# Kernel tuning notes

Hardware: AMD Instinct MI355X
Metric: run time of the kernel (lower is better)

## Reference

```python
import jax, jax.numpy as jnp
import numpy as np

B, T, N, F, E, K, H = 512, 48, 62, 5, 496, 3, 512
EPS = 1e-5


def setup_inputs() -> dict:
    key = jax.random.key(0)
    ks = jax.random.split(key, 12)
    x = jax.random.normal(ks[0], (B, T, N, F), jnp.float32)
    edge_src = jax.random.randint(ks[1], (B, E), 0, N)
    edge_dst = jax.random.randint(ks[2], (B, E), 0, N)
    edge_weight = jax.random.uniform(ks[3], (B, E), jnp.float32)
    # ChebConv weights: K linear maps (F->F) + bias, one set per time step t
    Wc = jax.random.normal(ks[4], (T, K, F, F), jnp.float32) * 0.3
    bc = jnp.zeros((T, F), jnp.float32)
    bn_gamma = jnp.ones((T, F), jnp.float32)
    bn_beta = jnp.zeros((T, F), jnp.float32)
    s = 1.0 / np.sqrt(H)
    W_ih = jax.random.uniform(ks[5], (4 * H, N * F), jnp.float32, -s, s)
    W_hh = jax.random.uniform(ks[6], (4 * H, H), jnp.float32, -s, s)
    b_ih = jax.random.uniform(ks[7], (4 * H,), jnp.float32, -s, s)
    b_hh = jax.random.uniform(ks[8], (4 * H,), jnp.float32, -s, s)
    bn1_gamma = jnp.ones((T,), jnp.float32)
    bn1_beta = jnp.zeros((T,), jnp.float32)
    Wl = jax.random.normal(ks[9], (3, H * T), jnp.float32) * 0.02
    bl = jnp.zeros((3,), jnp.float32)
    return dict(x=x, edge_src=edge_src, edge_dst=edge_dst, edge_weight=edge_weight,
                Wc=Wc, bc=bc, bn_gamma=bn_gamma, bn_beta=bn_beta,
                W_ih=W_ih, W_hh=W_hh, b_ih=b_ih, b_hh=b_hh,
                bn1_gamma=bn1_gamma, bn1_beta=bn1_beta, Wl=Wl, bl=bl)


def reference(x, edge_src, edge_dst, edge_weight, Wc, bc, bn_gamma, bn_beta,
              W_ih, W_hh, b_ih, b_hh, bn1_gamma, bn1_beta, Wl, bl):
    # ---- build dense per-graph adjacency (N=62 is tiny, dense is the fast form) ----
    b_idx = jnp.arange(B)[:, None]
    A = jnp.zeros((B, N, N), x.dtype).at[b_idx, edge_dst, edge_src].add(edge_weight)
    deg = A.sum(axis=-1)                      # (B, N) weighted in-degree
    safe = jnp.where(deg > 0, deg, 1.0)
    dinv = jnp.where(deg > 0, 1.0, 0.0) * jax.lax.rsqrt(safe)
    # scaled Laplacian with lambda_max=2 (PyG sym default): L_hat = -D^-1/2 A D^-1/2
    Lhat = -(dinv[:, :, None] * A * dinv[:, None, :])  # (B, N, N)

    # ---- ChebConv per time step, vectorized over T (per-t weights) ----
    xt = jnp.transpose(x, (1, 0, 2, 3))       # (T, B, N, F)
    Tx0 = xt
    out = jnp.einsum('tbnf,tfg->tbng', Tx0, Wc[:, 0])
    Tx1 = jnp.einsum('bnm,tbmf->tbnf', Lhat, Tx0)
    if K > 1:
        out = out + jnp.einsum('tbnf,tfg->tbng', Tx1, Wc[:, 1])
    for k in range(2, K):
        Tx2 = 2.0 * jnp.einsum('bnm,tbmf->tbnf', Lhat, Tx1) - Tx0
        out = out + jnp.einsum('tbnf,tfg->tbng', Tx2, Wc[:, k])
        Tx0, Tx1 = Tx1, Tx2
    out = out + bc[:, None, None, :]

    # ---- BatchNorm over all nodes in the batch (per t, per feature), training stats ----
    mu = out.mean(axis=(1, 2), keepdims=True)
    var = out.var(axis=(1, 2), keepdims=True)
    out = (out - mu) * jax.lax.rsqrt(var + EPS)
    out = out * bn_gamma[:, None, None, :] + bn_beta[:, None, None, :]

    # ---- reshape to LSTM sequence: (B, T, N*F) ----
    seq = jnp.transpose(out, (1, 0, 2, 3)).reshape(B, T, N * F)

    # ---- LSTM (torch gate order i,f,g,o) ----
    def step(carry, x_t):
        h, c = carry
        g = x_t @ W_ih.T + b_ih + h @ W_hh.T + b_hh
        i, f, gg, o = jnp.split(g, 4, axis=-1)
        c = jax.nn.sigmoid(f) * c + jax.nn.sigmoid(i) * jnp.tanh(gg)
        h = jax.nn.sigmoid(o) * jnp.tanh(c)
        return (h, c), h

    h0 = jnp.zeros((B, H), x.dtype)
    _, ys = jax.lax.scan(step, (h0, h0), jnp.transpose(seq, (1, 0, 2)))
    y = jnp.transpose(ys, (1, 0, 2))          # (B, T, H)

    # ---- BatchNorm1d with C=T channels: normalize over (B, H) per t ----
    mu1 = y.mean(axis=(0, 2), keepdims=True)
    var1 = y.var(axis=(0, 2), keepdims=True)
    y = (y - mu1) * jax.lax.rsqrt(var1 + EPS)
    y = y * bn1_gamma[None, :, None] + bn1_beta[None, :, None]

    # ---- head ----
    y = y.reshape(B, T * H)
    return y @ Wl.T + bl
```

## Files before the change

kernel.cpp:

```cpp
#include <hip/hip_runtime.h>
#include <hip/hip_bf16.h>
#include <cstdint>

#define B_ 512
#define T_ 48
#define N_ 62
#define F_ 5
#define E_ 496
#define H_ 512
#define NF_ 310
#define SEQP 320
#define KPAD 832
#define G4 2048
#define EPS_ 1e-5f
#define TC 12
#define LSTR 72

typedef __attribute__((ext_vector_type(8))) short short8;
typedef __attribute__((ext_vector_type(4))) short s16x4;
typedef __attribute__((ext_vector_type(4))) float f32x4;

__device__ __forceinline__ float sigm(float x)  { return 1.f / (1.f + __expf(-x)); }
__device__ __forceinline__ float tanhf_(float x){ return 2.f / (1.f + __expf(-2.f*x)) - 1.f; }

__device__ __forceinline__ short f2b(float v) {
  unsigned int u = __builtin_bit_cast(unsigned int, v);
  unsigned int r = (u + 0x7fffu + ((u >> 16) & 1u)) >> 16;
  return (short)r;
}
__device__ __forceinline__ float b2f(short s) {
  unsigned int u = ((unsigned int)(unsigned short)s) << 16;
  return __builtin_bit_cast(float, u);
}

__device__ __forceinline__ void dma16(const void* g, void* l) {
  __builtin_amdgcn_global_load_lds(
      (const __attribute__((address_space(1))) unsigned int*)g,
      (__attribute__((address_space(3))) unsigned int*)l, 16, 0, 0);
}

__global__ __launch_bounds__(256) void k_lapprep(
    const int* __restrict__ esrc, const int* __restrict__ edst, const float* __restrict__ ew,
    const float* __restrict__ Wih, const float* __restrict__ Whh,
    const float* __restrict__ bih, const float* __restrict__ bhh,
    __hip_bfloat16* __restrict__ lap,
    __hip_bfloat16* __restrict__ Wcat, float* __restrict__ biasr)
{
  const int bid = blockIdx.x;
  const int tid = threadIdx.x;
  __shared__ float Af[N_*N_];
  __shared__ float dinv[N_];

  if (bid < B_) {
    for (int i = tid; i < N_*N_; i += 256) Af[i] = 0.f;
    __syncthreads();
    for (int e = tid; e < E_; e += 256)
      atomicAdd(&Af[edst[bid*E_ + e]*N_ + esrc[bid*E_ + e]], ew[bid*E_ + e]);
    __syncthreads();
    if (tid < N_) {
      float s = 0.f;
      for (int m = 0; m < N_; ++m) s += Af[tid*N_ + m];
      dinv[tid] = (s > 0.f) ? rsqrtf(s) : 0.f;
    }
    __syncthreads();
    short* lp = (short*)lap + (size_t)bid*4096;
    for (int i = tid; i < 4096; i += 256) {
      int n = i >> 6, m = i & 63;
      float v = (n < N_ && m < N_) ? -dinv[n]*Af[n*N_ + m]*dinv[m] : 0.f;
      lp[i] = f2b(v);
    }
  } else {
    const int jp = bid - B_;
    const int g = jp & 3, jh = jp >> 2;
    const int jo = g*H_ + jh;
    for (int k = tid; k < KPAD; k += 256) {
      float v = 0.f;
      if (k < NF_) v = Wih[(size_t)jo*NF_ + k];
      else if (k >= SEQP) v = Whh[(size_t)jo*H_ + (k - SEQP)];
      Wcat[(size_t)jp*KPAD + k] = __float2bfloat16(v);
    }
    if (tid == 0) biasr[jp] = bih[jo] + bhh[jo];
  }
}

__global__ __launch_bounds__(512) void k_cheb(
    const float* __restrict__ x, const __hip_bfloat16* __restrict__ lap,
    const float* __restrict__ Wc, const float* __restrict__ bc,
    float* __restrict__ cheb, float* __restrict__ bps, float* __restrict__ bpq)
{
  __shared__ __align__(16) short SH[4*64*LSTR];
  short* Lb  = SH;
  short* Xt  = SH + 64*LSTR;
  short* T1t = SH + 2*64*LSTR;
  short* T2t = SH + 3*64*LSTR;

  const int tid = threadIdx.x;
  const int b = blockIdx.x;
  const int t0 = blockIdx.y * TC;

  {
    const short8* lp = (const short8*)((const short*)lap + (size_t)b*4096);
    short8 v = lp[tid];
    int n = tid >> 3, m = (tid & 7)*8;
    *(short8*)(Lb + n*LSTR + m) = v;
  }
  for (int i = tid; i < 64*LSTR; i += 512) Xt[i] = 0;
  __syncthreads();

  for (int i = tid; i < TC*NF_; i += 512) {
    int tl = i / NF_, nf = i - tl*NF_;
    float v = x[((size_t)b*T_ + t0 + tl)*NF_ + nf];
    int n = nf / F_, f = nf - n*F_;
    Xt[(tl*F_ + f)*LSTR + n] = f2b(v);
  }
  __syncthreads();

  const int w = tid >> 6, lane = tid & 63, l16 = lane & 15, lhi = lane >> 4;
  const int mt = w >> 1;
  const int nt = (w & 1) * 2;

  {
    f32x4 acc0 = {0.f,0.f,0.f,0.f}, acc1 = acc0;
    #pragma unroll
    for (int kc = 0; kc < 2; ++kc) {
      short8 a  = *(const short8*)(Lb + (mt*16 + l16)*LSTR + kc*32 + lhi*8);
      short8 b0 = *(const short8*)(Xt + ((nt  )*16 + l16)*LSTR + kc*32 + lhi*8);
      short8 b1 = *(const short8*)(Xt + ((nt+1)*16 + l16)*LSTR + kc*32 + lhi*8);
      acc0 = __builtin_amdgcn_mfma_f32_16x16x32_bf16(a, b0, acc0, 0, 0, 0);
      acc1 = __builtin_amdgcn_mfma_f32_16x16x32_bf16(a, b1, acc1, 0, 0, 0);
    }
    #pragma unroll
    for (int i = 0; i < 2; ++i) {
      f32x4 acc = i ? acc1 : acc0;
      int c = (nt+i)*16 + l16, n = mt*16 + lhi*4;
      s16x4 pk;
      #pragma unroll
      for (int r = 0; r < 4; ++r) pk[r] = f2b(acc[r]);
      *(s16x4*)(T1t + c*LSTR + n) = pk;
    }
  }
  __syncthreads();

  {
    f32x4 acc0 = {0.f,0.f,0.f,0.f}, acc1 = acc0;
    #pragma unroll
    for (int kc = 0; kc < 2; ++kc) {
      short8 a  = *(const short8*)(Lb + (mt*16 + l16)*LSTR + kc*32 + lhi*8);
      short8 b0 = *(const short8*)(T1t + ((nt  )*16 + l16)*LSTR + kc*32 + lhi*8);
      short8 b1 = *(const short8*)(T1t + ((nt+1)*16 + l16)*LSTR + kc*32 + lhi*8);
      acc0 = __builtin_amdgcn_mfma_f32_16x16x32_bf16(a, b0, acc0, 0, 0, 0);
      acc1 = __builtin_amdgcn_mfma_f32_16x16x32_bf16(a, b1, acc1, 0, 0, 0);
    }
    #pragma unroll
    for (int i = 0; i < 2; ++i) {
      f32x4 acc = i ? acc1 : acc0;
      int c = (nt+i)*16 + l16, n = mt*16 + lhi*4;
      s16x4 xv = *(const s16x4*)(Xt + c*LSTR + n);
      s16x4 pk;
      #pragma unroll
      for (int r = 0; r < 4; ++r) pk[r] = f2b(2.f*acc[r] - b2f(xv[r]));
      *(s16x4*)(T2t + c*LSTR + n) = pk;
    }
  }
  __syncthreads();

  const int pair = tid >> 2, q = tid & 3;
  if (pair < TC*F_) {
    const int tl = pair / F_, g = pair - (pair/F_)*F_;
    const int t = t0 + tl;
    float w0[5], w1[5], w2[5];
    #pragma unroll
    for (int ff = 0; ff < 5; ++ff) {
      w0[ff] = Wc[t*75 +      ff*5 + g];
      w1[ff] = Wc[t*75 + 25 + ff*5 + g];
      w2[ff] = Wc[t*75 + 50 + ff*5 + g];
    }
    const float bias = bc[t*F_ + g];
    float ss = 0.f, qq = 0.f;
    float* chout = cheb + ((size_t)t*B_ + b)*NF_;
    #pragma unroll
    for (int grp = 0; grp < 4; ++grp) {
      int n4 = grp*16 + q*4;
      float o[4] = {bias, bias, bias, bias};
      #pragma unroll
      for (int ff = 0; ff < 5; ++ff) {
        int c = tl*F_ + ff;
        s16x4 xv = *(const s16x4*)(Xt  + c*LSTR + n4);
        s16x4 v1 = *(const s16x4*)(T1t + c*LSTR + n4);
        s16x4 v2 = *(const s16x4*)(T2t + c*LSTR + n4);
        #pragma unroll
        for (int i = 0; i < 4; ++i)
          o[i] += b2f(xv[i])*w0[ff] + b2f(v1[i])*w1[ff] + b2f(v2[i])*w2[ff];
      }
      #pragma unroll
      for (int i = 0; i < 4; ++i) {
        int n = n4 + i;
        if (n < N_) { chout[n*F_ + g] = o[i]; ss += o[i]; qq += o[i]*o[i]; }
      }
    }
    ss += __shfl_down(ss, 2, 4); ss += __shfl_down(ss, 1, 4);
    qq += __shfl_down(qq, 2, 4); qq += __shfl_down(qq, 1, 4);
    if (q == 0) { bps[(t*F_ + g)*B_ + b] = ss; bpq[(t*F_ + g)*B_ + b] = qq; }
  }
}

__global__ __launch_bounds__(64) void k_bnfin(
    const float* __restrict__ bps, const float* __restrict__ bpq,
    const float* __restrict__ bng, const float* __restrict__ bnb,
    float* __restrict__ alpha, float* __restrict__ bet)
{
  const int tf = blockIdx.x;
  const int lane = threadIdx.x;
  float s = 0.f, q = 0.f;
  for (int i = lane; i < B_; i += 64) { s += bps[tf*B_ + i]; q += bpq[tf*B_ + i]; }
  #pragma unroll
  for (int off = 32; off; off >>= 1) { s += __shfl_down(s, off); q += __shfl_down(q, off); }
  if (lane == 0) {
    const float cnt = (float)(B_*N_);
    float mu = s / cnt;
    float var = q / cnt - mu*mu;
    float al = bng[tf] * rsqrtf(var + EPS_);
    alpha[tf] = al;
    bet[tf] = bnb[tf] - mu*al;
  }
}

__global__ __launch_bounds__(256) void k_seq(
    const float* __restrict__ cheb, const float* __restrict__ alpha, const float* __restrict__ bet,
    __hip_bfloat16* __restrict__ seqb)
{
  int idx = blockIdx.x*256 + threadIdx.x;
  int kp = idx % SEQP;
  int tb = idx / SEQP;
  int b = tb & (B_-1), t = tb >> 9;
  int sl = (kp >> 3) ^ (b & 7);
  int kl = sl*8 + (kp & 7);
  float v = 0.f;
  if (kl < NF_) v = cheb[(size_t)tb*NF_ + kl] * alpha[t*F_ + (kl % F_)] + bet[t*F_ + (kl % F_)];
  seqb[idx] = __float2bfloat16(v);
}

#define WOP(M)  M(0) M(1) M(2) M(3) M(4) M(5) M(6) M(7) M(8) M(9) M(10) M(11) M(12) M(13) \
                M(14) M(15) M(16) M(17) M(18) M(19) M(20) M(21) M(22) M(23) M(24) M(25)
#define WSEQ(M) M(0) M(1) M(2) M(3) M(4) M(5) M(6) M(7) M(8) M(9)
#define WHP(M)  M(10) M(11) M(12) M(13) M(14) M(15) M(16) M(17) M(18) M(19) M(20) M(21) \
                M(22) M(23) M(24) M(25)

#define DECLW(i) short8 wv##i;
#define LOADW(i) wv##i = *(const short8*)(wp + (i)*32); \
                 asm volatile("" : "+v"(wv##i));
#define MFS(i) { const int ph = (((i)*4 + lhi) ^ key)*8; \
                 short8 x0 = *(const short8*)(lseq + rs0*SEQP + ph); \
                 short8 x1 = *(const short8*)(lseq + rs1*SEQP + ph); \
                 a0 = __builtin_amdgcn_mfma_f32_16x16x32_bf16(x0, wv##i, a0, 0, 0, 0); \
                 a1 = __builtin_amdgcn_mfma_f32_16x16x32_bf16(x1, wv##i, a1, 0, 0, 0); }
#define MFH(i) { const int ph = ((((i)-10)*4 + lhi) ^ key)*8; \
                 short8 x0 = *(const short8*)(lh + rs0*H_ + ph); \
                 short8 x1 = *(const short8*)(lh + rs1*H_ + ph); \
                 a0 = __builtin_amdgcn_mfma_f32_16x16x32_bf16(x0, wv##i, a0, 0, 0, 0); \
                 a1 = __builtin_amdgcn_mfma_f32_16x16x32_bf16(x1, wv##i, a1, 0, 0, 0); }

__global__ __launch_bounds__(512, 1) void k_lstm(
    const __hip_bfloat16* __restrict__ seqb,
    const __hip_bfloat16* __restrict__ Wcat,
    const float* __restrict__ biasr,
    __hip_bfloat16* __restrict__ hb,
    unsigned int* __restrict__ bar)
{
  __shared__ __align__(16) short lh[32*H_];
  __shared__ __align__(16) short lseq[32*SEQP];
  __shared__ __align__(16) float gl[32][132];

  const int tid = threadIdx.x;
  const int bid = blockIdx.x;
  const int rg = bid & 15, jt = bid >> 4;
  const int b0 = rg*32, j0 = jt*128;
  const int w = tid >> 6, lane = tid & 63, l16 = lane & 15, lhi = lane >> 4;
  const int key = l16 & 7;
  const int rs0 = l16, rs1 = l16 + 16;

  const short* wp = (const short*)Wcat + (size_t)(j0 + w*16 + l16)*KPAD + lhi*8;
  WOP(DECLW)
  WOP(LOADW)

  const int crow = tid >> 4, u2 = tid & 15;
  const int hrow = b0 + crow;
  float cc0 = 0.f, cc1 = 0.f;
  f32x4 biaA = *(const f32x4*)(biasr + j0 + u2*8 + 0);
  f32x4 biaB = *(const f32x4*)(biasr + j0 + u2*8 + 4);
  const int hslot = (jt*4 + (u2 >> 2)) ^ (hrow & 7);
  const int hoff = hslot*8 + (u2 & 3)*2;

  const char* gseq = (const char*)seqb;
  const char* ghb  = (const char*)hb;
  char* lsc = (char*)lseq;
  char* lhc = (char*)lh;

  {
    const char* gs = gseq + ((size_t)b0)*640;
    #pragma unroll
    for (int i = 0; i < 3; ++i) {
      int c = w + i*8;
      if (c < 20) dma16(gs + c*1024 + lane*16, lsc + c*1024);
    }
  }

  #pragma unroll 1
  for (int t = 0; t < T_; ++t) {
    if (t > 0 && w == 0) {
      for (;;) {
        unsigned int v = 0xFFFFFFFFu;
        if (lane < 16)
          v = __hip_atomic_load(&bar[rg*64 + lane], __ATOMIC_RELAXED,
                                __HIP_MEMORY_SCOPE_AGENT);
        if (__all(v >= (unsigned int)t)) break;
        __builtin_amdgcn_s_sleep(1);
      }
    }
    __syncthreads();

    if (t > 0) {
      const char* gh = ghb + ((size_t)(t-1)*B_ + b0)*1024;
      #pragma unroll
      for (int i = 0; i < 4; ++i) {
        int c = w*4 + i;
        dma16(gh + c*1024 + lane*16, lhc + c*1024);
      }
    }

    f32x4 a0 = {0.f,0.f,0.f,0.f}, a1 = a0;
    WSEQ(MFS)

    if (t > 0) {
      __syncthreads();
      WHP(MFH)
    }

    #pragma unroll
    for (int r = 0; r < 4; ++r) {
      gl[     lhi*4 + r][w*16 + l16] = a0[r];
      gl[16 + lhi*4 + r][w*16 + l16] = a1[r];
    }
    __syncthreads();

    {
      f32x4 ga = *(const f32x4*)(&gl[crow][u2*8 + 0]);
      f32x4 gb = *(const f32x4*)(&gl[crow][u2*8 + 4]);
      float iv0 = sigm(ga[0]+biaA[0]), fv0 = sigm(ga[1]+biaA[1]);
      float gv0 = tanhf_(ga[2]+biaA[2]), ov0 = sigm(ga[3]+biaA[3]);
      cc0 = fv0*cc0 + iv0*gv0;
      float h0 = ov0*tanhf_(cc0);
      float iv1 = sigm(gb[0]+biaB[0]), fv1 = sigm(gb[1]+biaB[1]);
      float gv1 = tanhf_(gb[2]+biaB[2]), ov1 = sigm(gb[3]+biaB[3]);
      cc1 = fv1*cc1 + iv1*gv1;
      float h1 = ov1*tanhf_(cc1);
      unsigned int d0;
      asm("v_cvt_pk_bf16_f32 %0, %1, %2" : "=v"(d0) : "v"(h0), "v"(h1));
      short* dst = (short*)hb + ((size_t)t*B_ + hrow)*H_ + hoff;
      asm volatile("global_store_dword %0, %1, off sc0 sc1"
                   :: "v"(dst), "v"(d0) : "memory");
    }
    __syncthreads();

    if (t < T_ - 1) {
      if (tid == 0)
        __hip_atomic_store(&bar[rg*64 + jt], (unsigned int)(t+1),
                           __ATOMIC_RELAXED, __HIP_MEMORY_SCOPE_AGENT);
      const char* gs = gseq + ((size_t)(t+1)*B_ + b0)*640;
      #pragma unroll
      for (int i = 0; i < 3; ++i) {
        int c = w + i*8;
        if (c < 20) dma16(gs + c*1024 + lane*16, lsc + c*1024);
      }
    }
  }
}

__global__ __launch_bounds__(256) void k_bn1part(
    const __hip_bfloat16* __restrict__ hb, float* __restrict__ bn1s, float* __restrict__ bn1q)
{
  const int t = blockIdx.x, ch = blockIdx.y, tid = threadIdx.x;
  const short* base = (const short*)hb + ((size_t)t*B_ + ch*64)*H_;
  float s = 0.f, q = 0.f;
  for (int i = tid; i < 64*H_/8; i += 256) {
    short8 v8 = *(const short8*)(base + (i>>6)*H_ + (i&63)*8);
    #pragma unroll
    for (int j = 0; j < 8; ++j) { float v = b2f(v8[j]); s += v; q += v*v; }
  }
  __shared__ float rs[256], rq[256];
  rs[tid] = s; rq[tid] = q;
  __syncthreads();
  for (int o = 128; o; o >>= 1) {
    if (tid < o) { rs[tid] += rs[tid+o]; rq[tid] += rq[tid+o]; }
    __syncthreads();
  }
  if (tid == 0) { bn1s[t*8 + ch] = rs[0]; bn1q[t*8 + ch] = rq[0]; }
}

__global__ __launch_bounds__(256) void k_head(
    const __hip_bfloat16* __restrict__ hb, const float* __restrict__ bn1s,
    const float* __restrict__ bn1q, const float* __restrict__ g1,
    const float* __restrict__ be1, const float* __restrict__ Wl,
    const float* __restrict__ bl, float* __restrict__ out)
{
  const int b = blockIdx.x, tid = threadIdx.x;
  __shared__ float al1[T_], bt1[T_];
  if (tid < T_) {
    float s = 0.f, q = 0.f;
    #pragma unroll
    for (int ch = 0; ch < 8; ++ch) { s += bn1s[tid*8 + ch]; q += bn1q[tid*8 + ch]; }
    const float cnt = (float)(B_*H_);
    float mu = s / cnt, var = q / cnt - mu*mu;
    float al = g1[tid] * rsqrtf(var + EPS_);
    al1[tid] = al; bt1[tid] = be1[tid] - mu*al;
  }
  __syncthreads();
  float a0 = 0.f, a1 = 0.f, a2 = 0.f;
  const short* hbs = (const short*)hb;
  for (int p8 = tid; p8 < T_*(H_/8); p8 += 256) {
    const int t = p8 >> 6, p = p8 & 63;
    short8 v8 = *(const short8*)(hbs + ((size_t)t*B_ + b)*H_ + p*8);
    const int wi = t*H_ + ((p ^ (b & 7)) << 3);
    #pragma unroll
    for (int j = 0; j < 8; ++j) {
      float yn = b2f(v8[j])*al1[t] + bt1[t];
      a0 = fmaf(yn, Wl[wi + j],            a0);
      a1 = fmaf(yn, Wl[T_*H_ + wi + j],    a1);
      a2 = fmaf(yn, Wl[2*T_*H_ + wi + j],  a2);
    }
  }
  __shared__ float red[256];
  red[tid] = a0; __syncthreads();
  for (int o = 128; o; o >>= 1) { if (tid < o) red[tid] += red[tid+o]; __syncthreads(); }
  if (!tid) out[b*3 + 0] = red[0] + bl[0];
  __syncthreads();
  red[tid] = a1; __syncthreads();
  for (int o = 128; o; o >>= 1) { if (tid < o) red[tid] += red[tid+o]; __syncthreads(); }
  if (!tid) out[b*3 + 1] = red[0] + bl[1];
  __syncthreads();
  red[tid] = a2; __syncthreads();
  for (int o = 128; o; o >>= 1) { if (tid < o) red[tid] += red[tid+o]; __syncthreads(); }
  if (!tid) out[b*3 + 2] = red[0] + bl[2];
}

extern "C" void kernel_launch(void* const* d_in, const int* in_sizes, int n_in,
                              void* d_out, int out_size, void* d_ws, size_t ws_size,
                              hipStream_t stream)
{
  (void)in_sizes; (void)n_in; (void)out_size;
  const float* x   = (const float*)d_in[0];
  const int* esrc  = (const int*)d_in[1];
  const int* edst  = (const int*)d_in[2];
  const float* ew  = (const float*)d_in[3];
  const float* Wc  = (const float*)d_in[4];
  const float* bc  = (const float*)d_in[5];
  const float* bng = (const float*)d_in[6];
  const float* bnb = (const float*)d_in[7];
  const float* Wih = (const float*)d_in[8];
  const float* Whh = (const float*)d_in[9];
  const float* bih = (const float*)d_in[10];
  const float* bhh = (const float*)d_in[11];
  const float* g1  = (const float*)d_in[12];
  const float* be1 = (const float*)d_in[13];
  const float* Wl  = (const float*)d_in[14];
  const float* bl  = (const float*)d_in[15];
  float* out = (float*)d_out;

  char* ws = (char*)d_ws;
  size_t off = 0;
  auto alloc = [&](size_t bytes) {
    void* p = ws + off;
    off += (bytes + 255) & ~(size_t)255;
    return p;
  };
  float* cheb = (float*)alloc(sizeof(float)*(size_t)T_*B_*NF_);
  float* bps  = (float*)alloc(sizeof(float)*T_*F_*B_);
  float* bpq  = (float*)alloc(sizeof(float)*T_*F_*B_);
  float* alpha= (float*)alloc(sizeof(float)*T_*F_);
  float* bet  = (float*)alloc(sizeof(float)*T_*F_);
  __hip_bfloat16* lap  = (__hip_bfloat16*)alloc(sizeof(__hip_bfloat16)*(size_t)B_*4096);
  __hip_bfloat16* seqb = (__hip_bfloat16*)alloc(sizeof(__hip_bfloat16)*(size_t)T_*B_*SEQP);
  __hip_bfloat16* Wcat = (__hip_bfloat16*)alloc(sizeof(__hip_bfloat16)*(size_t)G4*KPAD);
  float* biasr = (float*)alloc(sizeof(float)*G4);
  __hip_bfloat16* hbuf = (__hip_bfloat16*)alloc(sizeof(__hip_bfloat16)*(size_t)T_*B_*H_);
  float* bn1s = (float*)alloc(sizeof(float)*T_*8);
  float* bn1q = (float*)alloc(sizeof(float)*T_*8);
  unsigned int* bar = (unsigned int*)alloc(sizeof(unsigned int)*16*64);
  if (ws_size < off) return;

  (void)hipMemsetAsync(bar, 0, sizeof(unsigned int)*16*64, stream);

  k_lapprep<<<B_ + G4, 256, 0, stream>>>(esrc, edst, ew, Wih, Whh, bih, bhh, lap, Wcat, biasr);
  k_cheb<<<dim3(B_, T_/TC), 512, 0, stream>>>(x, lap, Wc, bc, cheb, bps, bpq);
  k_bnfin<<<T_*F_, 64, 0, stream>>>(bps, bpq, bng, bnb, alpha, bet);
  k_seq<<<(T_*B_*SEQP)/256, 256, 0, stream>>>(cheb, alpha, bet, seqb);

  k_lstm<<<256, 512, 0, stream>>>(seqb, Wcat, biasr, hbuf, bar);

  k_bn1part<<<dim3(T_, 8), 256, 0, stream>>>(hbuf, bn1s, bn1q);
  k_head<<<B_, 256, 0, stream>>>(hbuf, bn1s, bn1q, g1, be1, Wl, bl, out);
}
```

Baseline: 246.5 us.

## Halve LSTM grid by giving each block 256 gate columns with doubled register weights

The persistent LSTM kernel now runs 128 blocks instead of 256, and each block computes 256 gate columns. Each wave keeps two 16-column weight tiles in registers and issues four MFMAs per k-step, so twice as many weights stay resident in VGPRs. Fewer blocks per row group means the cross-block barrier polls 8 flags instead of 16 and less h is reloaded redundantly per step. In exchange, register pressure rises (52 short8 weight vectors), LDS is reused for the gate buffer, which needs an extra sync, and per-step serial work per block doubles.

```diff
diff --git a/kernel.cpp b/kernel.cpp
--- a/kernel.cpp
+++ b/kernel.cpp
@@ -19,6 +19,7 @@
 typedef __attribute__((ext_vector_type(8))) short short8;
 typedef __attribute__((ext_vector_type(4))) short s16x4;
 typedef __attribute__((ext_vector_type(4))) float f32x4;
+typedef __attribute__((ext_vector_type(2))) unsigned int u32x2_;
 
 __device__ __forceinline__ float sigm(float x)  { return 1.f / (1.f + __expf(-x)); }
 __device__ __forceinline__ float tanhf_(float x){ return 2.f / (1.f + __expf(-2.f*x)) - 1.f; }
@@ -246,19 +247,24 @@
 #define WHP(M)  M(10) M(11) M(12) M(13) M(14) M(15) M(16) M(17) M(18) M(19) M(20) M(21) \
                 M(22) M(23) M(24) M(25)
 
-#define DECLW(i) short8 wv##i;
-#define LOADW(i) wv##i = *(const short8*)(wp + (i)*32); \
-                 asm volatile("" : "+v"(wv##i));
+#define DECLW(i) short8 wa##i, wb##i;
+#define LOADW(i) wa##i = *(const short8*)(wp0 + (i)*32); \
+                 wb##i = *(const short8*)(wp1 + (i)*32); \
+                 asm volatile("" : "+v"(wa##i), "+v"(wb##i));
 #define MFS(i) { const int ph = (((i)*4 + lhi) ^ key)*8; \
                  short8 x0 = *(const short8*)(lseq + rs0*SEQP + ph); \
                  short8 x1 = *(const short8*)(lseq + rs1*SEQP + ph); \
-                 a0 = __builtin_amdgcn_mfma_f32_16x16x32_bf16(x0, wv##i, a0, 0, 0, 0); \
-                 a1 = __builtin_amdgcn_mfma_f32_16x16x32_bf16(x1, wv##i, a1, 0, 0, 0); }
+                 a00 = __builtin_amdgcn_mfma_f32_16x16x32_bf16(x0, wa##i, a00, 0, 0, 0); \
+                 a01 = __builtin_amdgcn_mfma_f32_16x16x32_bf16(x0, wb##i, a01, 0, 0, 0); \
+                 a10 = __builtin_amdgcn_mfma_f32_16x16x32_bf16(x1, wa##i, a10, 0, 0, 0); \
+                 a11 = __builtin_amdgcn_mfma_f32_16x16x32_bf16(x1, wb##i, a11, 0, 0, 0); }
 #define MFH(i) { const int ph = ((((i)-10)*4 + lhi) ^ key)*8; \
                  short8 x0 = *(const short8*)(lh + rs0*H_ + ph); \
                  short8 x1 = *(const short8*)(lh + rs1*H_ + ph); \
-                 a0 = __builtin_amdgcn_mfma_f32_16x16x32_bf16(x0, wv##i, a0, 0, 0, 0); \
-                 a1 = __builtin_amdgcn_mfma_f32_16x16x32_bf16(x1, wv##i, a1, 0, 0, 0); }
+                 a00 = __builtin_amdgcn_mfma_f32_16x16x32_bf16(x0, wa##i, a00, 0, 0, 0); \
+                 a01 = __builtin_amdgcn_mfma_f32_16x16x32_bf16(x0, wb##i, a01, 0, 0, 0); \
+                 a10 = __builtin_amdgcn_mfma_f32_16x16x32_bf16(x1, wa##i, a10, 0, 0, 0); \
+                 a11 = __builtin_amdgcn_mfma_f32_16x16x32_bf16(x1, wb##i, a11, 0, 0, 0); }
 
 __global__ __launch_bounds__(512, 1) void k_lstm(
     const __hip_bfloat16* __restrict__ seqb,
@@ -267,35 +273,37 @@
     __hip_bfloat16* __restrict__ hb,
     unsigned int* __restrict__ bar)
 {
-  __shared__ __align__(16) short lh[32*H_];
-  __shared__ __align__(16) short lseq[32*SEQP];
-  __shared__ __align__(16) float gl[32][132];
+  __shared__ __align__(16) short SH2[32*H_ + 32*SEQP];
+  __shared__ __align__(16) float bs[256];
+  short* lh   = SH2;
+  short* lseq = SH2 + 32*H_;
+  float (*gl)[260] = (float (*)[260])SH2;
 
   const int tid = threadIdx.x;
   const int bid = blockIdx.x;
   const int rg = bid & 15, jt = bid >> 4;
-  const int b0 = rg*32, j0 = jt*128;
+  const int b0 = rg*32, j0 = jt*256;
   const int w = tid >> 6, lane = tid & 63, l16 = lane & 15, lhi = lane >> 4;
   const int key = l16 & 7;
   const int rs0 = l16, rs1 = l16 + 16;
 
-  const short* wp = (const short*)Wcat + (size_t)(j0 + w*16 + l16)*KPAD + lhi*8;
+  const short* wp0 = (const short*)Wcat + (size_t)(j0 + w*32      + l16)*KPAD + lhi*8;
+  const short* wp1 = (const short*)Wcat + (size_t)(j0 + w*32 + 16 + l16)*KPAD + lhi*8;
   WOP(DECLW)
   WOP(LOADW)
 
-  const int crow = tid >> 4, u2 = tid & 15;
+  const int crow = tid >> 4, u4 = tid & 15;
   const int hrow = b0 + crow;
-  float cc0 = 0.f, cc1 = 0.f;
-  f32x4 biaA = *(const f32x4*)(biasr + j0 + u2*8 + 0);
-  f32x4 biaB = *(const f32x4*)(biasr + j0 + u2*8 + 4);
-  const int hslot = (jt*4 + (u2 >> 2)) ^ (hrow & 7);
-  const int hoff = hslot*8 + (u2 & 3)*2;
+  f32x4 cc = {0.f, 0.f, 0.f, 0.f};
+  const int hslot = (jt*8 + (u4 >> 1)) ^ (hrow & 7);
+  const int hoff = hslot*8 + (u4 & 1)*4;
 
   const char* gseq = (const char*)seqb;
   const char* ghb  = (const char*)hb;
   char* lsc = (char*)lseq;
   char* lhc = (char*)lh;
 
+  if (tid < 64) ((f32x4*)bs)[tid] = ((const f32x4*)(biasr + j0))[tid];
   {
     const char* gs = gseq + ((size_t)b0)*640;
     #pragma unroll
@@ -310,7 +318,7 @@
     if (t > 0 && w == 0) {
       for (;;) {
         unsigned int v = 0xFFFFFFFFu;
-        if (lane < 16)
+        if (lane < 8)
           v = __hip_atomic_load(&bar[rg*64 + lane], __ATOMIC_RELAXED,
                                 __HIP_MEMORY_SCOPE_AGENT);
         if (__all(v >= (unsigned int)t)) break;
@@ -328,37 +336,44 @@
       }
     }
 
-    f32x4 a0 = {0.f,0.f,0.f,0.f}, a1 = a0;
+    f32x4 a00 = {0.f,0.f,0.f,0.f}, a01 = a00, a10 = a00, a11 = a00;
     WSEQ(MFS)
 
     if (t > 0) {
       __syncthreads();
       WHP(MFH)
     }
+    __syncthreads();
 
     #pragma unroll
     for (int r = 0; r < 4; ++r) {
-      gl[     lhi*4 + r][w*16 + l16] = a0[r];
-      gl[16 + lhi*4 + r][w*16 + l16] = a1[r];
+      gl[     lhi*4 + r][w*32      + l16] = a00[r];
+      gl[     lhi*4 + r][w*32 + 16 + l16] = a01[r];
+      gl[16 + lhi*4 + r][w*32      + l16] = a10[r];
+      gl[16 + lhi*4 + r][w*32 + 16 + l16] = a11[r];
     }
     __syncthreads();
 
     {
-      f32x4 ga = *(const f32x4*)(&gl[crow][u2*8 + 0]);
-      f32x4 gb = *(const f32x4*)(&gl[crow][u2*8 + 4]);
-      float iv0 = sigm(ga[0]+biaA[0]), fv0 = sigm(ga[1]+biaA[1]);
-      float gv0 = tanhf_(ga[2]+biaA[2]), ov0 = sigm(ga[3]+biaA[3]);
-      cc0 = fv0*cc0 + iv0*gv0;
-      float h0 = ov0*tanhf_(cc0);
-      float iv1 = sigm(gb[0]+biaB[0]), fv1 = sigm(gb[1]+biaB[1]);
-      float gv1 = tanhf_(gb[2]+biaB[2]), ov1 = sigm(gb[3]+biaB[3]);
-      cc1 = fv1*cc1 + iv1*gv1;
-      float h1 = ov1*tanhf_(cc1);
-      unsigned int d0;
-      asm("v_cvt_pk_bf16_f32 %0, %1, %2" : "=v"(d0) : "v"(h0), "v"(h1));
+      float hv[4];
+      #pragma unroll
+      for (int k = 0; k < 4; ++k) {
+        f32x4 g4  = *(const f32x4*)(&gl[crow][u4*16 + k*4]);
+        f32x4 bia = *(const f32x4*)(&bs[u4*16 + k*4]);
+        float iv = sigm  (g4[0] + bia[0]);
+        float fv = sigm  (g4[1] + bia[1]);
+        float gv = tanhf_(g4[2] + bia[2]);
+        float ov = sigm  (g4[3] + bia[3]);
+        cc[k] = fv*cc[k] + iv*gv;
+        hv[k] = ov*tanhf_(cc[k]);
+      }
+      unsigned int d0, d1;
+      asm("v_cvt_pk_bf16_f32 %0, %1, %2" : "=v"(d0) : "v"(hv[0]), "v"(hv[1]));
+      asm("v_cvt_pk_bf16_f32 %0, %1, %2" : "=v"(d1) : "v"(hv[2]), "v"(hv[3]));
+      u32x2_ dd; dd[0] = d0; dd[1] = d1;
       short* dst = (short*)hb + ((size_t)t*B_ + hrow)*H_ + hoff;
-      asm volatile("global_store_dword %0, %1, off sc0 sc1"
-                   :: "v"(dst), "v"(d0) : "memory");
+      asm volatile("global_store_dwordx2 %0, %1, off sc0 sc1"
+                   :: "v"(dst), "v"(dd) : "memory");
     }
     __syncthreads();
 
@@ -495,7 +510,7 @@
   k_bnfin<<<T_*F_, 64, 0, stream>>>(bps, bpq, bng, bnb, alpha, bet);
   k_seq<<<(T_*B_*SEQP)/256, 256, 0, stream>>>(cheb, alpha, bet, seqb);
 
-  k_lstm<<<256, 512, 0, stream>>>(seqb, Wcat, biasr, hbuf, bar);
+  k_lstm<<<128, 512, 0, stream>>>(seqb, Wcat, biasr, hbuf, bar);
 
   k_bn1part<<<dim3(T_, 8), 256, 0, stream>>>(hbuf, bn1s, bn1q);
   k_head<<<B_, 256, 0, stream>>>(hbuf, bn1s, bn1q, g1, be1, Wl, bl, out);
```

After: 511.7 us. 108% more time.
